# Optimization experiments

Measured on AMD Instinct MI355X. Metric: run time of the kernel, lower is better.

The kernel has to match this reference:

```python
import jax, jax.numpy as jnp
import numpy as np

M, K, D = 8, 4096, 128
N, H, W = 8, 64, 64


def setup_inputs() -> dict:
    key = jax.random.key(0)
    k1, k2, k3, k4 = jax.random.split(key, 4)
    codes = jax.random.randint(k1, (N, H, W, M), 0, K, dtype=jnp.int64)
    codebook = jax.random.normal(k2, (M, K, D), dtype=jnp.float32)
    wq = jax.random.normal(k3, (M, D, D), dtype=jnp.float32) / jnp.sqrt(jnp.float32(D))
    bq = jax.random.normal(k4, (M, D), dtype=jnp.float32) * 0.01
    return {"codes": codes, "codebook": codebook, "wq": wq, "bq": bq}


def reference(codes, codebook, wq, bq):
    n, h, w, m = codes.shape
    # gather: indexed[n,h,w,m,d] = codebook[m_idx, codes[n,h,w,m_idx]]
    ix = jnp.arange(m)  # broadcasts against codes' last dim
    indexed = codebook[ix, codes]  # [n,h,w,m,d]
    # per-group small matmul + bias
    out = jnp.einsum('nhwmd,mcd->nhwmc', indexed, wq) + bq  # [n,h,w,m,d]
    return out.reshape(n, h, w, -1).transpose(0, 3, 1, 2)  # [n, m*d, h, w]
```

## Files before the change

### kernel.cpp

```cpp
#include <hip/hip_runtime.h>
#include <hip/hip_bf16.h>

#define PM 8
#define PK 4096
#define PD 128
#define PN 8
#define PH 64
#define PW 64

typedef __attribute__((ext_vector_type(8))) short bf16x8;
typedef __attribute__((ext_vector_type(4))) float f32x4;
typedef __attribute__((ext_vector_type(8))) short short8v;

__device__ inline unsigned short f2bf_rne(float f) {
    unsigned int u = __float_as_uint(f);
    unsigned int r = (u + 0x7FFFu + ((u >> 16) & 1u)) >> 16;
    return (unsigned short)r;
}
__device__ inline float bf2f(unsigned short s) {
    return __uint_as_float(((unsigned int)s) << 16);
}

__device__ inline bf16x8 loadcvt8(const float* __restrict__ p) {
    f32x4 x0 = *(const f32x4*)p;
    f32x4 x1 = *(const f32x4*)(p + 4);
    bf16x8 r;
#pragma unroll
    for (int j = 0; j < 4; ++j) {
        r[j]     = (short)f2bf_rne(x0[j]);
        r[j + 4] = (short)f2bf_rne(x1[j]);
    }
    return r;
}

__global__ __launch_bounds__(256) void build_table(
        const float* __restrict__ codebook,
        const float* __restrict__ wq,
        const float* __restrict__ bq,
        unsigned short* __restrict__ table) {
    const int b = blockIdx.x;
    const int m = b & 7;
    const int ktile = (b >> 3) * 128;
    const int tid = threadIdx.x;
    const int wv = tid >> 6;
    const int l  = tid & 63;
    const int lr = l & 15;
    const int lg = l >> 4;

    const float* cb = codebook + (size_t)m * PK * PD;
    const float* wm = wq + (size_t)m * PD * PD;

    bf16x8 afrag[2][4];
#pragma unroll
    for (int ks = 0; ks < 2; ++ks) {
        const int k = ktile + wv * 32 + ks * 16 + lr;
        const float* src = cb + (size_t)k * PD + lg * 8;
#pragma unroll
        for (int kk = 0; kk < 4; ++kk) {
            afrag[ks][kk] = loadcvt8(src + kk * 32);
        }
    }

#pragma unroll
    for (int cs = 0; cs < 8; ++cs) {
        const int c = cs * 16 + lr;
        bf16x8 bfrag[4];
        const float* src = wm + (size_t)c * PD + lg * 8;
#pragma unroll
        for (int kk = 0; kk < 4; ++kk) {
            bfrag[kk] = loadcvt8(src + kk * 32);
        }
        const float bias = bq[m * PD + c];
#pragma unroll
        for (int ks = 0; ks < 2; ++ks) {
            f32x4 acc = {0.f, 0.f, 0.f, 0.f};
#pragma unroll
            for (int kk = 0; kk < 4; ++kk) {
                acc = __builtin_amdgcn_mfma_f32_16x16x32_bf16(
                        afrag[ks][kk], bfrag[kk], acc, 0, 0, 0);
            }
            const int kb = ktile + wv * 32 + ks * 16 + lg * 4;
            unsigned short* dst = table + ((size_t)(m * PK + kb)) * PD + cs * 16 + lr;
#pragma unroll
            for (int j = 0; j < 4; ++j) {
                dst[(size_t)j * PD] = f2bf_rne(acc[j] + bias);
            }
        }
    }
}

__global__ __launch_bounds__(256) void gather_scatter(
        const int* __restrict__ codes,
        const unsigned short* __restrict__ table,
        float* __restrict__ out) {
    const int b = blockIdx.x;
    const int m = b & 7;
    const int rest = b >> 3;
    const int n = rest >> 6;
    const int h = rest & 63;
    const int tid = threadIdx.x;
    const int w = tid & 63;
    const int cb0 = (tid >> 6) * 32;

    const int code = codes[((n * PH + h) * PW + w) * PM + m];
    const unsigned short* row = table + ((size_t)m * PK + code) * PD + cb0;
    float* ob = out + (((size_t)n * (PM * PD) + m * PD + cb0) * PH + h) * PW + w;

#pragma unroll
    for (int i = 0; i < 4; ++i) {
        short8v v = *(const short8v*)(row + i * 8);
#pragma unroll
        for (int j = 0; j < 8; ++j) {
            __builtin_nontemporal_store(bf2f((unsigned short)v[j]),
                                        ob + (size_t)(i * 8 + j) * (PH * PW));
        }
    }
}

__global__ __launch_bounds__(256) void fused_direct(
        const int* __restrict__ codes,
        const float* __restrict__ codebook,
        const float* __restrict__ wq,
        const float* __restrict__ bq,
        float* __restrict__ out) {
    __shared__ float rows[PW][133];
    const int b = blockIdx.x;
    const int m = b & 7;
    const int rest = b >> 3;
    const int n = rest >> 6;
    const int h = rest & 63;
    const int tid = threadIdx.x;

    for (int idx = tid; idx < PW * 32; idx += 256) {
        const int r = idx >> 5;
        const int e = (idx & 31) * 4;
        const int code = codes[((n * PH + h) * PW + r) * PM + m];
        const float* src = codebook + ((size_t)m * PK + code) * PD + e;
#pragma unroll
        for (int j = 0; j < 4; ++j) rows[r][e + j] = src[j];
    }
    __syncthreads();

    const int w = tid & 63;
    const int cb0 = (tid >> 6) * 32;
    float* ob = out + (((size_t)n * (PM * PD) + m * PD + cb0) * PH + h) * PW + w;
    for (int ci = 0; ci < 32; ++ci) {
        const int c = cb0 + ci;
        const float* wr = wq + ((size_t)m * PD + c) * PD;
        float acc = bq[m * PD + c];
#pragma unroll 4
        for (int d = 0; d < PD; ++d) acc += rows[w][d] * wr[d];
        ob[(size_t)ci * (PH * PW)] = acc;
    }
}

extern "C" void kernel_launch(void* const* d_in, const int* in_sizes, int n_in,
                              void* d_out, int out_size, void* d_ws, size_t ws_size,
                              hipStream_t stream) {
    const int*   codes    = (const int*)  d_in[0];
    const float* codebook = (const float*)d_in[1];
    const float* wq       = (const float*)d_in[2];
    const float* bq       = (const float*)d_in[3];
    float* out = (float*)d_out;

    const size_t table_bytes = (size_t)PM * PK * PD * sizeof(unsigned short);
    if (ws_size >= table_bytes) {
        unsigned short* table = (unsigned short*)d_ws;
        build_table<<<dim3(256), dim3(256), 0, stream>>>(codebook, wq, bq, table);
        gather_scatter<<<dim3(PM * PN * PH), dim3(256), 0, stream>>>(codes, table, out);
    } else {
        fused_direct<<<dim3(PM * PN * PH), dim3(256), 0, stream>>>(codes, codebook, wq, bq, out);
    }
}
```

Before: 41.83 us.

## Vectorize gather_scatter stores over four w positions and halve build_table tiles

The gather kernel now has each thread handle four consecutive w positions for 32 channels, so it writes 16-byte f32x4 nontemporal stores instead of scalar stores. It also reads four table rows per thread, and the grid is remapped to 1024 blocks covering h-groups and channel-groups. build_table now processes 64 codes per block with 512 blocks, trading per-block work for more parallelism across CUs. Per-thread register use for the raw loads rises, and each lane's table reads are less coalesced across the wave.

```diff
diff --git a/kernel.cpp b/kernel.cpp
--- a/kernel.cpp
+++ b/kernel.cpp
@@ -40,7 +40,7 @@
         unsigned short* __restrict__ table) {
     const int b = blockIdx.x;
     const int m = b & 7;
-    const int ktile = (b >> 3) * 128;
+    const int ktile = (b >> 3) * 64;
     const int tid = threadIdx.x;
     const int wv = tid >> 6;
     const int l  = tid & 63;
@@ -50,15 +50,12 @@
     const float* cb = codebook + (size_t)m * PK * PD;
     const float* wm = wq + (size_t)m * PD * PD;
 
-    bf16x8 afrag[2][4];
+    const int k = ktile + wv * 16 + lr;
+    const float* asrc = cb + (size_t)k * PD + lg * 8;
+    bf16x8 afrag[4];
 #pragma unroll
-    for (int ks = 0; ks < 2; ++ks) {
-        const int k = ktile + wv * 32 + ks * 16 + lr;
-        const float* src = cb + (size_t)k * PD + lg * 8;
-#pragma unroll
-        for (int kk = 0; kk < 4; ++kk) {
-            afrag[ks][kk] = loadcvt8(src + kk * 32);
-        }
+    for (int kk = 0; kk < 4; ++kk) {
+        afrag[kk] = loadcvt8(asrc + kk * 32);
     }
 
 #pragma unroll
@@ -71,20 +68,17 @@
             bfrag[kk] = loadcvt8(src + kk * 32);
         }
         const float bias = bq[m * PD + c];
+        f32x4 acc = {0.f, 0.f, 0.f, 0.f};
 #pragma unroll
-        for (int ks = 0; ks < 2; ++ks) {
-            f32x4 acc = {0.f, 0.f, 0.f, 0.f};
+        for (int kk = 0; kk < 4; ++kk) {
+            acc = __builtin_amdgcn_mfma_f32_16x16x32_bf16(
+                    afrag[kk], bfrag[kk], acc, 0, 0, 0);
+        }
+        const int kb = ktile + wv * 16 + lg * 4;
+        unsigned short* dst = table + ((size_t)(m * PK + kb)) * PD + cs * 16 + lr;
 #pragma unroll
-            for (int kk = 0; kk < 4; ++kk) {
-                acc = __builtin_amdgcn_mfma_f32_16x16x32_bf16(
-                        afrag[ks][kk], bfrag[kk], acc, 0, 0, 0);
-            }
-            const int kb = ktile + wv * 32 + ks * 16 + lg * 4;
-            unsigned short* dst = table + ((size_t)(m * PK + kb)) * PD + cs * 16 + lr;
-#pragma unroll
-            for (int j = 0; j < 4; ++j) {
-                dst[(size_t)j * PD] = f2bf_rne(acc[j] + bias);
-            }
+        for (int j = 0; j < 4; ++j) {
+            dst[(size_t)j * PD] = f2bf_rne(acc[j] + bias);
         }
     }
 }
@@ -94,25 +88,51 @@
         const unsigned short* __restrict__ table,
         float* __restrict__ out) {
     const int b = blockIdx.x;
-    const int m = b & 7;
-    const int rest = b >> 3;
-    const int n = rest >> 6;
-    const int h = rest & 63;
+    const int m  = b & 7;
+    const int r  = b >> 3;
+    const int hg = r & 3;
+    const int cg = (r >> 2) & 3;
+    const int n  = r >> 4;
     const int tid = threadIdx.x;
-    const int w = tid & 63;
-    const int cb0 = (tid >> 6) * 32;
+    const int wv = tid >> 6;
+    const int l  = tid & 63;
 
-    const int code = codes[((n * PH + h) * PW + w) * PM + m];
-    const unsigned short* row = table + ((size_t)m * PK + code) * PD + cb0;
-    float* ob = out + (((size_t)n * (PM * PD) + m * PD + cb0) * PH + h) * PW + w;
+    const int h  = hg * 16 + wv * 4 + (l >> 4);
+    const int w0 = (l & 15) * 4;
+    const int c0 = cg * 32;
 
+    const int* cbase = codes + ((size_t)(n * PH + h) * PW + w0) * PM + m;
+    int code0 = cbase[0 * PM];
+    int code1 = cbase[1 * PM];
+    int code2 = cbase[2 * PM];
+    int code3 = cbase[3 * PM];
+
+    const unsigned short* trow0 = table + ((size_t)m * PK + code0) * PD + c0;
+    const unsigned short* trow1 = table + ((size_t)m * PK + code1) * PD + c0;
+    const unsigned short* trow2 = table + ((size_t)m * PK + code2) * PD + c0;
+    const unsigned short* trow3 = table + ((size_t)m * PK + code3) * PD + c0;
+
+    short8v raw0[4], raw1[4], raw2[4], raw3[4];
 #pragma unroll
-    for (int i = 0; i < 4; ++i) {
-        short8v v = *(const short8v*)(row + i * 8);
+    for (int ci = 0; ci < 4; ++ci) {
+        raw0[ci] = *(const short8v*)(trow0 + ci * 8);
+        raw1[ci] = *(const short8v*)(trow1 + ci * 8);
+        raw2[ci] = *(const short8v*)(trow2 + ci * 8);
+        raw3[ci] = *(const short8v*)(trow3 + ci * 8);
+    }
+
+    float* ob = out + (((size_t)n * (PM * PD) + m * PD + c0) * PH + h) * PW + w0;
+#pragma unroll
+    for (int ci = 0; ci < 4; ++ci) {
 #pragma unroll
         for (int j = 0; j < 8; ++j) {
-            __builtin_nontemporal_store(bf2f((unsigned short)v[j]),
-                                        ob + (size_t)(i * 8 + j) * (PH * PW));
+            const int c = ci * 8 + j;
+            f32x4 v;
+            v[0] = bf2f((unsigned short)raw0[ci][j]);
+            v[1] = bf2f((unsigned short)raw1[ci][j]);
+            v[2] = bf2f((unsigned short)raw2[ci][j]);
+            v[3] = bf2f((unsigned short)raw3[ci][j]);
+            __builtin_nontemporal_store(v, (f32x4*)(ob + (size_t)c * (PH * PW)));
         }
     }
 }
@@ -166,8 +186,8 @@
     const size_t table_bytes = (size_t)PM * PK * PD * sizeof(unsigned short);
     if (ws_size >= table_bytes) {
         unsigned short* table = (unsigned short*)d_ws;
-        build_table<<<dim3(256), dim3(256), 0, stream>>>(codebook, wq, bq, table);
-        gather_scatter<<<dim3(PM * PN * PH), dim3(256), 0, stream>>>(codes, table, out);
+        build_table<<<dim3(512), dim3(256), 0, stream>>>(codebook, wq, bq, table);
+        gather_scatter<<<dim3(1024), dim3(256), 0, stream>>>(codes, table, out);
     } else {
         fused_direct<<<dim3(PM * PN * PH), dim3(256), 0, stream>>>(codes, codebook, wq, bq, out);
     }
```

Result: slower. 53.73 us (+28.5%).

## Split table build over output halves and remap gather to two pixels per lane

Applied to the files above, without the earlier changes.

The table-building kernel now splits each k-tile's output columns into two halves, doubling the grid to 512 blocks for more parallelism at the cost of reloading the codebook fragments twice. The gather kernel is remapped so each lane handles two adjacent w positions and 32 channels, loading both table rows up front and emitting 8-byte vectorized nontemporal stores. It also adds a launch-bounds occupancy hint. The aim is better memory-level parallelism and fewer, wider store instructions for the large output write.

```diff
diff --git a/kernel.cpp b/kernel.cpp
--- a/kernel.cpp
+++ b/kernel.cpp
@@ -10,6 +10,7 @@
 
 typedef __attribute__((ext_vector_type(8))) short bf16x8;
 typedef __attribute__((ext_vector_type(4))) float f32x4;
+typedef __attribute__((ext_vector_type(2))) float f32x2;
 typedef __attribute__((ext_vector_type(8))) short short8v;
 
 __device__ inline unsigned short f2bf_rne(float f) {
@@ -40,7 +41,9 @@
         unsigned short* __restrict__ table) {
     const int b = blockIdx.x;
     const int m = b & 7;
-    const int ktile = (b >> 3) * 128;
+    const int r = b >> 3;
+    const int ktile = (r & 31) * 128;
+    const int cshalf = r >> 5;
     const int tid = threadIdx.x;
     const int wv = tid >> 6;
     const int l  = tid & 63;
@@ -62,7 +65,8 @@
     }
 
 #pragma unroll
-    for (int cs = 0; cs < 8; ++cs) {
+    for (int i = 0; i < 4; ++i) {
+        const int cs = cshalf * 4 + i;
         const int c = cs * 16 + lr;
         bf16x8 bfrag[4];
         const float* src = wm + (size_t)c * PD + lg * 8;
@@ -89,30 +93,49 @@
     }
 }
 
-__global__ __launch_bounds__(256) void gather_scatter(
+__global__ __launch_bounds__(256, 4) void gather_scatter(
         const int* __restrict__ codes,
         const unsigned short* __restrict__ table,
         float* __restrict__ out) {
     const int b = blockIdx.x;
-    const int m = b & 7;
-    const int rest = b >> 3;
-    const int n = rest >> 6;
-    const int h = rest & 63;
+    const int m  = b & 7;
+    const int r  = b >> 3;
+    const int hg = r & 7;
+    const int cg = (r >> 3) & 3;
+    const int n  = r >> 5;
     const int tid = threadIdx.x;
-    const int w = tid & 63;
-    const int cb0 = (tid >> 6) * 32;
+    const int wv = tid >> 6;
+    const int l  = tid & 63;
 
-    const int code = codes[((n * PH + h) * PW + w) * PM + m];
-    const unsigned short* row = table + ((size_t)m * PK + code) * PD + cb0;
-    float* ob = out + (((size_t)n * (PM * PD) + m * PD + cb0) * PH + h) * PW + w;
+    const int hh = l >> 5;
+    const int h  = hg * 8 + wv * 2 + hh;
+    const int w0 = (l & 31) * 2;
+    const int c0 = cg * 32;
 
+    const int* cbase = codes + ((size_t)(n * PH + h) * PW + w0) * PM + m;
+    const int code0 = cbase[0];
+    const int code1 = cbase[PM];
+
+    const unsigned short* trow0 = table + ((size_t)m * PK + code0) * PD + c0;
+    const unsigned short* trow1 = table + ((size_t)m * PK + code1) * PD + c0;
+
+    short8v raw0[4], raw1[4];
 #pragma unroll
-    for (int i = 0; i < 4; ++i) {
-        short8v v = *(const short8v*)(row + i * 8);
+    for (int ci = 0; ci < 4; ++ci) {
+        raw0[ci] = *(const short8v*)(trow0 + ci * 8);
+        raw1[ci] = *(const short8v*)(trow1 + ci * 8);
+    }
+
+    float* ob = out + (((size_t)n * (PM * PD) + m * PD + c0) * PH + h) * PW + w0;
+#pragma unroll
+    for (int ci = 0; ci < 4; ++ci) {
 #pragma unroll
         for (int j = 0; j < 8; ++j) {
-            __builtin_nontemporal_store(bf2f((unsigned short)v[j]),
-                                        ob + (size_t)(i * 8 + j) * (PH * PW));
+            const int c = ci * 8 + j;
+            f32x2 v;
+            v[0] = bf2f((unsigned short)raw0[ci][j]);
+            v[1] = bf2f((unsigned short)raw1[ci][j]);
+            __builtin_nontemporal_store(v, (f32x2*)(ob + (size_t)c * (PH * PW)));
         }
     }
 }
@@ -166,8 +189,8 @@
     const size_t table_bytes = (size_t)PM * PK * PD * sizeof(unsigned short);
     if (ws_size >= table_bytes) {
         unsigned short* table = (unsigned short*)d_ws;
-        build_table<<<dim3(256), dim3(256), 0, stream>>>(codebook, wq, bq, table);
-        gather_scatter<<<dim3(PM * PN * PH), dim3(256), 0, stream>>>(codes, table, out);
+        build_table<<<dim3(512), dim3(256), 0, stream>>>(codebook, wq, bq, table);
+        gather_scatter<<<dim3(2048), dim3(256), 0, stream>>>(codes, table, out);
     } else {
         fused_direct<<<dim3(PM * PN * PH), dim3(256), 0, stream>>>(codes, codebook, wq, bq, out);
     }
```

After: 43.58 us. 1.04x slower.

## Stage wq in LDS, swap MFMA operands for packed table stores, drop nontemporal stores

Applied to the files above, without the earlier changes.

build_table now converts each group's wq matrix to bf16 once per block and stages it in shared memory, and stages the bias there too. Each wave then reads wq fragments from LDS instead of re-reading and re-converting them from global memory. Swapping the MFMA operand roles leaves each lane holding four consecutive output columns of one table row, so it writes an 8-byte packed store instead of four scattered 2-byte stores. The gather_scatter kernel also goes back from nontemporal stores to ordinary stores for the output. The cost is a block-level barrier and extra LDS use in the table builder.

```diff
diff --git a/kernel.cpp b/kernel.cpp
--- a/kernel.cpp
+++ b/kernel.cpp
@@ -38,9 +38,11 @@
         const float* __restrict__ wq,
         const float* __restrict__ bq,
         unsigned short* __restrict__ table) {
+    __shared__ unsigned short ldsA[2048 * 8];
+    __shared__ float lds_bq[PD];
     const int b = blockIdx.x;
     const int m = b & 7;
-    const int ktile = (b >> 3) * 128;
+    const int kt0 = (b >> 3) * 128;
     const int tid = threadIdx.x;
     const int wv = tid >> 6;
     const int l  = tid & 63;
@@ -50,41 +52,58 @@
     const float* cb = codebook + (size_t)m * PK * PD;
     const float* wm = wq + (size_t)m * PD * PD;
 
-    bf16x8 afrag[2][4];
+    if (tid < PD) lds_bq[tid] = bq[m * PD + tid];
+
+    {
+        const int lr_s = tid & 15;
+        const int u0 = (tid >> 4) * 8;
+#pragma unroll
+        for (int i = 0; i < 8; ++i) {
+            const int u  = u0 + i;
+            const int cs = u >> 4;
+            const int kk = (u >> 2) & 3;
+            const int lgs = u & 3;
+            bf16x8 v = loadcvt8(wm + (size_t)(cs * 16 + lr_s) * PD + kk * 32 + lgs * 8);
+            *(bf16x8*)&ldsA[(size_t)(u * 16 + lr_s) * 8] = v;
+        }
+    }
+
+    bf16x8 bfragc[2][4];
 #pragma unroll
     for (int ks = 0; ks < 2; ++ks) {
-        const int k = ktile + wv * 32 + ks * 16 + lr;
+        const int k = kt0 + wv * 32 + ks * 16 + lr;
         const float* src = cb + (size_t)k * PD + lg * 8;
 #pragma unroll
         for (int kk = 0; kk < 4; ++kk) {
-            afrag[ks][kk] = loadcvt8(src + kk * 32);
+            bfragc[ks][kk] = loadcvt8(src + kk * 32);
         }
     }
+    __syncthreads();
 
 #pragma unroll
     for (int cs = 0; cs < 8; ++cs) {
-        const int c = cs * 16 + lr;
-        bf16x8 bfrag[4];
-        const float* src = wm + (size_t)c * PD + lg * 8;
+        bf16x8 afragw[4];
 #pragma unroll
         for (int kk = 0; kk < 4; ++kk) {
-            bfrag[kk] = loadcvt8(src + kk * 32);
+            const int u = (cs << 4) | (kk << 2) | lg;
+            afragw[kk] = *(const bf16x8*)&ldsA[(size_t)(u * 16 + lr) * 8];
         }
-        const float bias = bq[m * PD + c];
+        const f32x4 bias4 = *(const f32x4*)&lds_bq[cs * 16 + lg * 4];
 #pragma unroll
         for (int ks = 0; ks < 2; ++ks) {
             f32x4 acc = {0.f, 0.f, 0.f, 0.f};
 #pragma unroll
             for (int kk = 0; kk < 4; ++kk) {
                 acc = __builtin_amdgcn_mfma_f32_16x16x32_bf16(
-                        afrag[ks][kk], bfrag[kk], acc, 0, 0, 0);
+                        afragw[kk], bfragc[ks][kk], acc, 0, 0, 0);
             }
-            const int kb = ktile + wv * 32 + ks * 16 + lg * 4;
-            unsigned short* dst = table + ((size_t)(m * PK + kb)) * PD + cs * 16 + lr;
-#pragma unroll
-            for (int j = 0; j < 4; ++j) {
-                dst[(size_t)j * PD] = f2bf_rne(acc[j] + bias);
-            }
+            const int k = kt0 + wv * 32 + ks * 16 + lr;
+            unsigned int p0 = (unsigned int)f2bf_rne(acc[0] + bias4[0])
+                            | ((unsigned int)f2bf_rne(acc[1] + bias4[1]) << 16);
+            unsigned int p1 = (unsigned int)f2bf_rne(acc[2] + bias4[2])
+                            | ((unsigned int)f2bf_rne(acc[3] + bias4[3]) << 16);
+            uint2 pk; pk.x = p0; pk.y = p1;
+            *(uint2*)&table[((size_t)(m * PK + k)) * PD + cs * 16 + lg * 4] = pk;
         }
     }
 }
@@ -111,8 +130,7 @@
         short8v v = *(const short8v*)(row + i * 8);
 #pragma unroll
         for (int j = 0; j < 8; ++j) {
-            __builtin_nontemporal_store(bf2f((unsigned short)v[j]),
-                                        ob + (size_t)(i * 8 + j) * (PH * PW));
+            ob[(size_t)(i * 8 + j) * (PH * PW)] = bf2f((unsigned short)v[j]);
         }
     }
 }
```

After: 37.41 us, median of 2. 1.12x faster.
